# Optimization experiments

Measured on AMD Instinct MI355X. Metric: run time of the kernel, lower is better.

## Reference

```python
import jax, jax.numpy as jnp
import numpy as np
import math

E_IN, E_OUT = 512, 96
B, QL, PL = 64, 128, 196

def _lin(k, shape):
    fan_in = shape[1]
    bound = 1.0 / math.sqrt(fan_in)
    k1, k2 = jax.random.split(k)
    W = jax.random.uniform(k1, shape, jnp.float32, -bound, bound)
    b = jax.random.uniform(k2, (shape[0],), jnp.float32, -bound, bound)
    return W, b

def setup_inputs() -> dict:
    key = jax.random.key(0)
    ks = jax.random.split(key, 16)
    inp = {
        'z_d_cls': jax.random.normal(ks[0], (B, E_IN), jnp.float32),
        'Z_d_tok': jax.random.normal(ks[1], (B, QL, E_IN), jnp.float32),
        'z_t_cls': jax.random.normal(ks[2], (B, E_IN), jnp.float32),
        'Z_t_tok': jax.random.normal(ks[3], (B, QL, E_IN), jnp.float32),
        'z_v_cls': jax.random.normal(ks[4], (B, E_IN), jnp.float32),
        'Z_v_patch': jax.random.normal(ks[5], (B, PL, E_IN), jnp.float32),
    }
    names = ['t_cls', 'd_cls', 'v_cls', 't_tok', 'v_patch', 'tgl_q', 'tgl_k', 'tgl_v']
    for i, n in enumerate(names):
        W, b = _lin(ks[6 + i], (E_OUT, E_IN))
        inp[f'W_{n}'] = W
        inp[f'b_{n}'] = b
    inp['ln_g'] = jnp.ones((E_OUT,), jnp.float32)
    inp['ln_b'] = jnp.zeros((E_OUT,), jnp.float32)
    return inp

def _l2n(x, eps=1e-6):
    return x / jnp.maximum(jnp.linalg.norm(x, axis=-1, keepdims=True), eps)

def _proj(x, W, b):
    return x @ W.T + b

def _layer_norm(x, g, b, eps=1e-5):
    mu = jnp.mean(x, axis=-1, keepdims=True)
    var = jnp.mean((x - mu) ** 2, axis=-1, keepdims=True)
    return (x - mu) / jnp.sqrt(var + eps) * g + b

def reference(z_d_cls, Z_d_tok, z_t_cls, Z_t_tok, z_v_cls, Z_v_patch,
              W_t_cls, b_t_cls, W_d_cls, b_d_cls, W_v_cls, b_v_cls,
              W_t_tok, b_t_tok, W_v_patch, b_v_patch,
              W_tgl_q, b_tgl_q, W_tgl_k, b_tgl_k, W_tgl_v, b_tgl_v,
              ln_g, ln_b):
    # --- TGG: global-global text/doc cosine sim [B, B]
    t = _l2n(_proj(z_t_cls, W_t_cls, b_t_cls))
    d = _l2n(_proj(z_d_cls, W_d_cls, b_d_cls))
    S_TGG = t @ d.T
    # --- TGL: cross-attention over all batch pairs
    Q = _proj(Z_d_tok, W_tgl_q, b_tgl_q)   # [b, q, h]
    K = _proj(Z_t_tok, W_tgl_k, b_tgl_k)   # [c, k, h]
    V = _proj(Z_t_tok, W_tgl_v, b_tgl_v)   # [c, k, h]
    scores = jnp.einsum('bqh,ckh->bcqk', Q, K) / math.sqrt(E_OUT)
    attn = jax.nn.softmax(scores, axis=-1)
    context = jnp.einsum('bcqk,ckh->bcqh', attn, V).mean(axis=2)  # [b, c, h]
    context = _layer_norm(context, ln_g, ln_b)
    S_TGL = jnp.einsum('ih,ijh->ij', d, _l2n(context))
    S_TIB = 0.5 * (S_TGG + S_TGL)
    # --- CGG: global-global text/vision cosine sim
    v = _l2n(_proj(z_v_cls, W_v_cls, b_v_cls))
    S_CGG = t @ v.T
    # --- CLL: token-patch max similarity
    t_tok = _l2n(_proj(Z_t_tok, W_t_tok, b_t_tok))        # [b, t, h]
    v_pat = _l2n(_proj(Z_v_patch, W_v_patch, b_v_patch))  # [c, p, h]
    sim = jnp.einsum('bth,cph->bctp', t_tok, v_pat)
    S_CLL = sim.max(axis=(-1, -2))
    S_CAB = 0.5 * (S_CGG + S_CLL)
    return S_TIB + S_CAB
```

## Files before the change

### kernel.cpp

```cpp
#include <hip/hip_runtime.h>
#include <hip/hip_bf16.h>

typedef __bf16 bf16;
typedef __attribute__((ext_vector_type(8))) __bf16 bf16x8;
typedef __attribute__((ext_vector_type(4))) float f32x4;
typedef __attribute__((ext_vector_type(4))) unsigned int uint4v;

#define MFMA16(a, b, c) __builtin_amdgcn_mfma_f32_16x16x32_bf16(a, b, c, 0, 0, 0)

__device__ inline bf16x8 cvt8(const float* p) {
    f32x4 lo = *(const f32x4*)p;
    f32x4 hi = *(const f32x4*)(p + 4);
    bf16x8 r;
    r[0] = (bf16)lo[0]; r[1] = (bf16)lo[1]; r[2] = (bf16)lo[2]; r[3] = (bf16)lo[3];
    r[4] = (bf16)hi[0]; r[5] = (bf16)hi[1]; r[6] = (bf16)hi[2]; r[7] = (bf16)hi[3];
    return r;
}


struct WPtrs { const float* W[8]; };

__global__ __launch_bounds__(256) void cvtw_kernel(WPtrs wp, bf16* __restrict__ Wb) {
    int j   = blockIdx.x / 48;
    int blk = blockIdx.x - j * 48;
    int idx = (blk * 256 + threadIdx.x) * 4;
    f32x4 v = *(const f32x4*)(wp.W[j] + idx);
    bf16* dst = Wb + j * 49152 + idx;
    dst[0] = (bf16)v[0]; dst[1] = (bf16)v[1]; dst[2] = (bf16)v[2]; dst[3] = (bf16)v[3];
}


struct ProjParams {
    const float* src[8];
    const float* B[8];
    void* dst[8];
    const bf16* Wb;
};

__global__ __launch_bounds__(128, 8) void proj_kernel(ProjParams p) {
    int g   = blockIdx.x;
    int tid = threadIdx.x;
    int nh = tid >> 6, lane = tid & 63;
    int m = lane & 15, quad = lane >> 4;

    int job = 0, base = 0;
    if (g >= 2)    { job = 1; base = 2; }
    if (g >= 4)    { job = 2; base = 4; }
    if (g >= 6)    { job = 3; base = 6; }
    if (g >= 262)  { job = 4; base = 262; }
    if (g >= 518)  { job = 5; base = 518; }
    if (g >= 774)  { job = 6; base = 774; }
    if (g >= 1030) { job = 7; base = 1030; }
    int r0 = (g - base) << 5;

    const float* X  = p.src[job];
    const bf16*  wb = p.Wb + job * 49152 + (size_t)(nh * 48 + m) * 512 + quad * 8;
    const float* x0 = X + (size_t)(r0 + m) * 512 + quad * 8;
    const float* x1 = x0 + 16 * 512;

    f32x4 acc[2][3] = {};
    #pragma unroll 4
    for (int kk = 0; kk < 512; kk += 32) {
        bf16x8 a0 = cvt8(x0 + kk);
        bf16x8 a1 = cvt8(x1 + kk);
        #pragma unroll
        for (int nt = 0; nt < 3; nt++) {
            bf16x8 b = *(const bf16x8*)(wb + nt * 8192 + kk);
            acc[0][nt] = MFMA16(a0, b, acc[0][nt]);
            acc[1][nt] = MFMA16(a1, b, acc[1][nt]);
        }
    }
    const float* Bv = p.B[job];
    #pragma unroll
    for (int t2 = 0; t2 < 2; t2++)
        #pragma unroll
        for (int nt = 0; nt < 3; nt++) {
            float bb = Bv[nh * 48 + nt * 16 + m];
            acc[t2][nt][0] += bb; acc[t2][nt][1] += bb;
            acc[t2][nt][2] += bb; acc[t2][nt][3] += bb;
        }

    bool norm = (job < 3) || (job >= 6);
    __shared__ float sx[2][2][16];
    if (norm) {
        float ss[2][4];
        #pragma unroll
        for (int t2 = 0; t2 < 2; t2++)
            #pragma unroll
            for (int r = 0; r < 4; r++) {
                float s = 0.0f;
                #pragma unroll
                for (int nt = 0; nt < 3; nt++) s += acc[t2][nt][r] * acc[t2][nt][r];
                s += __shfl_xor(s, 1); s += __shfl_xor(s, 2);
                s += __shfl_xor(s, 4); s += __shfl_xor(s, 8);
                ss[t2][r] = s;
            }
        if (m == 0) {
            #pragma unroll
            for (int t2 = 0; t2 < 2; t2++)
                #pragma unroll
                for (int r = 0; r < 4; r++)
                    sx[nh][t2][quad * 4 + r] = ss[t2][r];
        }
        __syncthreads();
        #pragma unroll
        for (int t2 = 0; t2 < 2; t2++)
            #pragma unroll
            for (int r = 0; r < 4; r++) {
                float tot = ss[t2][r] + sx[1 - nh][t2][quad * 4 + r];
                float inv = 1.0f / fmaxf(sqrtf(tot), 1e-6f);
                #pragma unroll
                for (int nt = 0; nt < 3; nt++) acc[t2][nt][r] *= inv;
            }
    }
    if (job < 3) {
        float* dst = (float*)p.dst[job];
        #pragma unroll
        for (int t2 = 0; t2 < 2; t2++)
            #pragma unroll
            for (int r = 0; r < 4; r++)
                #pragma unroll
                for (int nt = 0; nt < 3; nt++)
                    dst[(size_t)(r0 + t2 * 16 + quad * 4 + r) * 96 + nh * 48 + nt * 16 + m] = acc[t2][nt][r];
    } else {
        bf16* dst = (bf16*)p.dst[job];
        #pragma unroll
        for (int t2 = 0; t2 < 2; t2++)
            #pragma unroll
            for (int r = 0; r < 4; r++)
                #pragma unroll
                for (int nt = 0; nt < 3; nt++)
                    dst[(size_t)(r0 + t2 * 16 + quad * 4 + r) * 96 + nh * 48 + nt * 16 + m] = (bf16)acc[t2][nt][r];
    }
}


__global__ __launch_bounds__(256) void attn_kernel(
    const bf16* __restrict__ Qg, const bf16* __restrict__ Kg, const bf16* __restrict__ Vg,
    const float* __restrict__ dvec, const float* __restrict__ ln_g, const float* __restrict__ ln_b,
    float* __restrict__ S_TGL)
{
    int b = blockIdx.x >> 6, c = blockIdx.x & 63;
    int tid = threadIdx.x, lane = tid & 63, w = tid >> 6;
    int m = lane & 15, quad = lane >> 4;
    const bf16* Q = Qg + (size_t)b * (128 * 96);
    const bf16* K = Kg + (size_t)c * (128 * 96);
    const bf16* V = Vg + (size_t)c * (128 * 96);

    __shared__ __align__(16) bf16 Klds[128 * 104];
    #pragma unroll
    for (int it = 0; it < 6; it++) {
        int ch = it * 256 + tid;
        int row = ch / 12, seg = ch - row * 12;
        *(uint4v*)(Klds + row * 104 + seg * 8) = *(const uint4v*)(K + ch * 8);
    }
    __syncthreads();

    f32x4 acc[2][8] = {};
    #pragma unroll
    for (int kk = 0; kk < 96; kk += 32) {
        bf16x8 a0 = *(const bf16x8*)(Q + (size_t)(w * 32 + m) * 96 + kk + quad * 8);
        bf16x8 a1 = *(const bf16x8*)(Q + (size_t)(w * 32 + 16 + m) * 96 + kk + quad * 8);
        #pragma unroll
        for (int nt = 0; nt < 8; nt++) {
            bf16x8 bb = *(const bf16x8*)(Klds + (nt * 16 + m) * 104 + kk + quad * 8);
            acc[0][nt] = MFMA16(a0, bb, acc[0][nt]);
            acc[1][nt] = MFMA16(a1, bb, acc[1][nt]);
        }
    }
    const float sc = 0.10206207261596575f;
    float wpart[8];
    #pragma unroll
    for (int nt = 0; nt < 8; nt++) wpart[nt] = 0.0f;
    #pragma unroll
    for (int mt = 0; mt < 2; mt++) {
        #pragma unroll
        for (int r = 0; r < 4; r++) {
            float tv[8]; float mx = -3.4e38f;
            #pragma unroll
            for (int nt = 0; nt < 8; nt++) { tv[nt] = acc[mt][nt][r] * sc; mx = fmaxf(mx, tv[nt]); }
            mx = fmaxf(mx, __shfl_xor(mx, 1)); mx = fmaxf(mx, __shfl_xor(mx, 2));
            mx = fmaxf(mx, __shfl_xor(mx, 4)); mx = fmaxf(mx, __shfl_xor(mx, 8));
            float s = 0.0f;
            #pragma unroll
            for (int nt = 0; nt < 8; nt++) { tv[nt] = __expf(tv[nt] - mx); s += tv[nt]; }
            s += __shfl_xor(s, 1); s += __shfl_xor(s, 2);
            s += __shfl_xor(s, 4); s += __shfl_xor(s, 8);
            float inv = 1.0f / s;
            #pragma unroll
            for (int nt = 0; nt < 8; nt++) wpart[nt] += tv[nt] * inv;
        }
    }
    #pragma unroll
    for (int nt = 0; nt < 8; nt++) {
        wpart[nt] += __shfl_xor(wpart[nt], 16);
        wpart[nt] += __shfl_xor(wpart[nt], 32);
    }
    __shared__ float wsum4[4][128];
    __shared__ float wk[128];
    __shared__ float ctxp[4][96];
    __shared__ float ctx[96];
    if (lane < 16) {
        #pragma unroll
        for (int nt = 0; nt < 8; nt++) wsum4[w][nt * 16 + lane] = wpart[nt];
    }
    __syncthreads();
    if (tid < 128) wk[tid] = wsum4[0][tid] + wsum4[1][tid] + wsum4[2][tid] + wsum4[3][tid];
    __syncthreads();
    {
        float c0 = 0.0f, c1 = 0.0f;
        if (lane < 48) {
            #pragma unroll 4
            for (int r = 0; r < 32; r++) {
                int k = w * 32 + r;
                unsigned u = *(const unsigned*)(V + (size_t)k * 96 + lane * 2);
                float lo = __uint_as_float(u << 16);
                float hi = __uint_as_float(u & 0xffff0000u);
                float wkk = wk[k];
                c0 += wkk * lo; c1 += wkk * hi;
            }
            ctxp[w][lane * 2]     = c0;
            ctxp[w][lane * 2 + 1] = c1;
        }
    }
    __syncthreads();
    if (tid < 96) ctx[tid] = (ctxp[0][tid] + ctxp[1][tid] + ctxp[2][tid] + ctxp[3][tid]) * (1.0f / 128.0f);
    __syncthreads();
    if (w == 0) {
        float x0 = ctx[lane];
        float x1 = (lane < 32) ? ctx[64 + lane] : 0.0f;
        float s = x0 + x1;
        #pragma unroll
        for (int d = 1; d < 64; d <<= 1) s += __shfl_xor(s, d);
        float mean = s * (1.0f / 96.0f);
        float e0 = x0 - mean;
        float e1 = (lane < 32) ? (x1 - mean) : 0.0f;
        float q = e0 * e0 + e1 * e1;
        #pragma unroll
        for (int d = 1; d < 64; d <<= 1) q += __shfl_xor(q, d);
        float rstd = rsqrtf(q * (1.0f / 96.0f) + 1e-5f);
        float y0 = e0 * rstd * ln_g[lane] + ln_b[lane];
        float y1 = 0.0f;
        if (lane < 32) y1 = e1 * rstd * ln_g[64 + lane] + ln_b[64 + lane];
        const float* db = dvec + b * 96;
        float dot = y0 * db[lane] + ((lane < 32) ? y1 * db[64 + lane] : 0.0f);
        float ss = y0 * y0 + y1 * y1;
        #pragma unroll
        for (int d = 1; d < 64; d <<= 1) { dot += __shfl_xor(dot, d); ss += __shfl_xor(ss, d); }
        if (lane == 0) S_TGL[blockIdx.x] = dot / fmaxf(sqrtf(ss), 1e-6f);
    }
}


__global__ __launch_bounds__(256) void cll_kernel(
    const bf16* __restrict__ Tt, const bf16* __restrict__ Vp, float* __restrict__ S_CLL)
{
    int b = blockIdx.x >> 6, c = blockIdx.x & 63;
    int tid = threadIdx.x, lane = tid & 63, w = tid >> 6;
    int m = lane & 15, quad = lane >> 4;
    const bf16* T = Tt + (size_t)b * (128 * 96);
    const bf16* P = Vp + (size_t)c * (196 * 96);

    __shared__ __align__(16) bf16 Plds[196 * 104];
    for (int ch = tid; ch < 2352; ch += 256) {
        int row = ch / 12, seg = ch - row * 12;
        *(uint4v*)(Plds + row * 104 + seg * 8) = *(const uint4v*)(P + ch * 8);
    }
    __syncthreads();

    int rofs[13];
    #pragma unroll
    for (int nt = 0; nt < 13; nt++) {
        int r = nt * 16 + m; if (r > 195) r = 195;
        rofs[nt] = r * 104;
    }
    f32x4 acc[2][13] = {};
    #pragma unroll
    for (int kk = 0; kk < 96; kk += 32) {
        bf16x8 a0 = *(const bf16x8*)(T + (size_t)(w * 32 + m) * 96 + kk + quad * 8);
        bf16x8 a1 = *(const bf16x8*)(T + (size_t)(w * 32 + 16 + m) * 96 + kk + quad * 8);
        #pragma unroll
        for (int nt = 0; nt < 13; nt++) {
            bf16x8 bb = *(const bf16x8*)(Plds + rofs[nt] + kk + quad * 8);
            acc[0][nt] = MFMA16(a0, bb, acc[0][nt]);
            acc[1][nt] = MFMA16(a1, bb, acc[1][nt]);
        }
    }
    float mx = -3.4e38f;
    #pragma unroll
    for (int mt = 0; mt < 2; mt++)
        #pragma unroll
        for (int nt = 0; nt < 13; nt++)
            #pragma unroll
            for (int r = 0; r < 4; r++) mx = fmaxf(mx, acc[mt][nt][r]);
    #pragma unroll
    for (int d = 1; d < 64; d <<= 1) mx = fmaxf(mx, __shfl_xor(mx, d));
    __shared__ float red[4];
    if (lane == 0) red[w] = mx;
    __syncthreads();
    if (tid == 0) S_CLL[blockIdx.x] = fmaxf(fmaxf(red[0], red[1]), fmaxf(red[2], red[3]));
}


__global__ __launch_bounds__(64) void final_kernel(
    const float* __restrict__ t, const float* __restrict__ d, const float* __restrict__ v,
    const float* __restrict__ S_TGL, const float* __restrict__ S_CLL, float* __restrict__ out)
{
    int i = blockIdx.x, j = threadIdx.x;
    __shared__ float ti[96];
    if (j < 64) ti[j] = t[i * 96 + j];
    if (j < 32) ti[64 + j] = t[i * 96 + 64 + j];
    __syncthreads();
    float tg = 0.0f, cg = 0.0f;
    const float* dj = d + j * 96;
    const float* vj = v + j * 96;
    #pragma unroll 8
    for (int h = 0; h < 96; h++) { float th = ti[h]; tg += th * dj[h]; cg += th * vj[h]; }
    float res = 0.5f * (tg + S_TGL[i * 64 + j]) + 0.5f * (cg + S_CLL[i * 64 + j]);
    out[i * 64 + j] = res;
}


extern "C" void kernel_launch(void* const* d_in, const int* in_sizes, int n_in,
                              void* d_out, int out_size, void* d_ws, size_t ws_size,
                              hipStream_t stream)
{
    (void)in_sizes; (void)n_in; (void)out_size; (void)ws_size;
    const float* z_d_cls   = (const float*)d_in[0];
    const float* Z_d_tok   = (const float*)d_in[1];
    const float* z_t_cls   = (const float*)d_in[2];
    const float* Z_t_tok   = (const float*)d_in[3];
    const float* z_v_cls   = (const float*)d_in[4];
    const float* Z_v_patch = (const float*)d_in[5];

    char* ws = (char*)d_ws;
    float* t     = (float*)(ws + 0);
    float* d     = (float*)(ws + 24576);
    float* v     = (float*)(ws + 49152);
    float* S_TGL = (float*)(ws + 73728);
    float* S_CLL = (float*)(ws + 90112);
    bf16* Wb = (bf16*)(ws + 106496);
    bf16* Qb = (bf16*)(ws + 892928);
    bf16* Kb = (bf16*)(ws + 892928 + 1572864);
    bf16* Vb = (bf16*)(ws + 892928 + 2 * 1572864);
    bf16* Tt = (bf16*)(ws + 892928 + 3 * 1572864);
    bf16* Vp = (bf16*)(ws + 892928 + 4 * 1572864);

    WPtrs wp;
    wp.W[0] = (const float*)d_in[6];
    wp.W[1] = (const float*)d_in[8];
    wp.W[2] = (const float*)d_in[10];
    wp.W[3] = (const float*)d_in[16];
    wp.W[4] = (const float*)d_in[18];
    wp.W[5] = (const float*)d_in[20];
    wp.W[6] = (const float*)d_in[12];
    wp.W[7] = (const float*)d_in[14];
    hipLaunchKernelGGL(cvtw_kernel, dim3(384), dim3(256), 0, stream, wp, Wb);

    ProjParams pp;
    pp.Wb = Wb;
    pp.src[0] = z_t_cls;   pp.B[0] = (const float*)d_in[7];  pp.dst[0] = t;
    pp.src[1] = z_d_cls;   pp.B[1] = (const float*)d_in[9];  pp.dst[1] = d;
    pp.src[2] = z_v_cls;   pp.B[2] = (const float*)d_in[11]; pp.dst[2] = v;
    pp.src[3] = Z_d_tok;   pp.B[3] = (const float*)d_in[17]; pp.dst[3] = Qb;
    pp.src[4] = Z_t_tok;   pp.B[4] = (const float*)d_in[19]; pp.dst[4] = Kb;
    pp.src[5] = Z_t_tok;   pp.B[5] = (const float*)d_in[21]; pp.dst[5] = Vb;
    pp.src[6] = Z_t_tok;   pp.B[6] = (const float*)d_in[13]; pp.dst[6] = Tt;
    pp.src[7] = Z_v_patch; pp.B[7] = (const float*)d_in[15]; pp.dst[7] = Vp;
    hipLaunchKernelGGL(proj_kernel, dim3(1422), dim3(128), 0, stream, pp);

    hipLaunchKernelGGL(attn_kernel, dim3(4096), dim3(256), 0, stream,
                       (const bf16*)Qb, (const bf16*)Kb, (const bf16*)Vb,
                       (const float*)d, (const float*)d_in[22], (const float*)d_in[23], S_TGL);
    hipLaunchKernelGGL(cll_kernel, dim3(4096), dim3(256), 0, stream,
                       (const bf16*)Tt, (const bf16*)Vp, S_CLL);
    hipLaunchKernelGGL(final_kernel, dim3(64), dim3(64), 0, stream,
                       (const float*)t, (const float*)d, (const float*)v,
                       (const float*)S_TGL, (const float*)S_CLL, (float*)d_out);
}
```

Measured before the change: 243.9 us.

## Fuse K/V/token projections, fold softmax scale into Q, merge attention and CLL

The three projections of Z_t_tok (K, V and the token projection) now run in one block that converts each input tile once and reuses it for all three weight sets. This cuts repeated global reads and fp32-to-bf16 conversions of the largest input. The softmax scale and log2(e) are folded into Q at projection time, so the attention softmax uses exp2 with no max subtraction. The attention and CLL kernels are merged into one 8192-block launch, with even and odd blocks taking each role and sharing a shared-memory union. Skipping the max subtraction relies on scores staying small enough not to overflow, and the fused K/V/T path uses more registers.

```diff
diff --git a/kernel.cpp b/kernel.cpp
--- a/kernel.cpp
+++ b/kernel.cpp
@@ -1,5 +1,6 @@
 #include <hip/hip_runtime.h>
 #include <hip/hip_bf16.h>
+#include <math.h>
 
 typedef __bf16 bf16;
 typedef __attribute__((ext_vector_type(8))) __bf16 bf16x8;
@@ -7,6 +8,8 @@
 typedef __attribute__((ext_vector_type(4))) unsigned int uint4v;
 
 #define MFMA16(a, b, c) __builtin_amdgcn_mfma_f32_16x16x32_bf16(a, b, c, 0, 0, 0)
+
+#define QSCALE 0.14724450f
 
 __device__ inline bf16x8 cvt8(const float* p) {
     f32x4 lo = *(const f32x4*)p;
@@ -31,58 +34,147 @@
 
 
 struct ProjParams {
-    const float* src[8];
-    const float* B[8];
-    void* dst[8];
+    const float* z_t_cls; const float* z_d_cls; const float* z_v_cls;
+    const float* Z_d_tok; const float* Z_t_tok; const float* Z_v_patch;
+    const float* b_t; const float* b_d; const float* b_v;
+    const float* b_q; const float* b_k; const float* b_vv; const float* b_tt; const float* b_vp;
+    float *t, *d, *v;
+    bf16 *Qb, *Kb, *Vb, *Tt, *Vp;
     const bf16* Wb;
 };
 
-__global__ __launch_bounds__(128, 8) void proj_kernel(ProjParams p) {
+__global__ __launch_bounds__(128, 3) void proj_kernel(ProjParams p) {
     int g   = blockIdx.x;
     int tid = threadIdx.x;
     int nh = tid >> 6, lane = tid & 63;
     int m = lane & 15, quad = lane >> 4;
 
-    int job = 0, base = 0;
-    if (g >= 2)    { job = 1; base = 2; }
-    if (g >= 4)    { job = 2; base = 4; }
-    if (g >= 6)    { job = 3; base = 6; }
-    if (g >= 262)  { job = 4; base = 262; }
-    if (g >= 518)  { job = 5; base = 518; }
-    if (g >= 774)  { job = 6; base = 774; }
-    if (g >= 1030) { job = 7; base = 1030; }
+    int job, base;
+    if (g < 2)        { job = 0; base = 0; }
+    else if (g < 4)   { job = 1; base = 2; }
+    else if (g < 6)   { job = 2; base = 4; }
+    else if (g < 262) { job = 3; base = 6; }
+    else if (g < 518) { job = 4; base = 262; }
+    else              { job = 5; base = 518; }
     int r0 = (g - base) << 5;
 
-    const float* X  = p.src[job];
-    const bf16*  wb = p.Wb + job * 49152 + (size_t)(nh * 48 + m) * 512 + quad * 8;
+    const float* X = (job == 0) ? p.z_t_cls : (job == 1) ? p.z_d_cls : (job == 2) ? p.z_v_cls
+                   : (job == 3) ? p.Z_d_tok : (job == 4) ? p.Z_t_tok : p.Z_v_patch;
     const float* x0 = X + (size_t)(r0 + m) * 512 + quad * 8;
     const float* x1 = x0 + 16 * 512;
 
-    f32x4 acc[2][3] = {};
-    #pragma unroll 4
-    for (int kk = 0; kk < 512; kk += 32) {
-        bf16x8 a0 = cvt8(x0 + kk);
-        bf16x8 a1 = cvt8(x1 + kk);
-        #pragma unroll
-        for (int nt = 0; nt < 3; nt++) {
-            bf16x8 b = *(const bf16x8*)(wb + nt * 8192 + kk);
-            acc[0][nt] = MFMA16(a0, b, acc[0][nt]);
-            acc[1][nt] = MFMA16(a1, b, acc[1][nt]);
-        }
-    }
-    const float* Bv = p.B[job];
-    #pragma unroll
-    for (int t2 = 0; t2 < 2; t2++)
-        #pragma unroll
-        for (int nt = 0; nt < 3; nt++) {
-            float bb = Bv[nh * 48 + nt * 16 + m];
-            acc[t2][nt][0] += bb; acc[t2][nt][1] += bb;
-            acc[t2][nt][2] += bb; acc[t2][nt][3] += bb;
-        }
-
-    bool norm = (job < 3) || (job >= 6);
     __shared__ float sx[2][2][16];
-    if (norm) {
+
+    if (job != 4) {
+        int jw = (job < 4) ? job : 7;
+        const bf16* wb = p.Wb + jw * 49152 + (size_t)(nh * 48 + m) * 512 + quad * 8;
+        f32x4 acc[2][3] = {};
+        #pragma unroll 4
+        for (int kk = 0; kk < 512; kk += 32) {
+            bf16x8 a0 = cvt8(x0 + kk);
+            bf16x8 a1 = cvt8(x1 + kk);
+            #pragma unroll
+            for (int nt = 0; nt < 3; nt++) {
+                bf16x8 b = *(const bf16x8*)(wb + nt * 8192 + kk);
+                acc[0][nt] = MFMA16(a0, b, acc[0][nt]);
+                acc[1][nt] = MFMA16(a1, b, acc[1][nt]);
+            }
+        }
+        const float* Bv = (job == 0) ? p.b_t : (job == 1) ? p.b_d : (job == 2) ? p.b_v
+                        : (job == 3) ? p.b_q : p.b_vp;
+        #pragma unroll
+        for (int t2 = 0; t2 < 2; t2++)
+            #pragma unroll
+            for (int nt = 0; nt < 3; nt++) {
+                float bb = Bv[nh * 48 + nt * 16 + m];
+                acc[t2][nt][0] += bb; acc[t2][nt][1] += bb;
+                acc[t2][nt][2] += bb; acc[t2][nt][3] += bb;
+            }
+        bool norm = (job != 3);
+        if (norm) {
+            float ss[2][4];
+            #pragma unroll
+            for (int t2 = 0; t2 < 2; t2++)
+                #pragma unroll
+                for (int r = 0; r < 4; r++) {
+                    float s = 0.0f;
+                    #pragma unroll
+                    for (int nt = 0; nt < 3; nt++) s += acc[t2][nt][r] * acc[t2][nt][r];
+                    s += __shfl_xor(s, 1); s += __shfl_xor(s, 2);
+                    s += __shfl_xor(s, 4); s += __shfl_xor(s, 8);
+                    ss[t2][r] = s;
+                }
+            if (m == 0)
+                #pragma unroll
+                for (int t2 = 0; t2 < 2; t2++)
+                    #pragma unroll
+                    for (int r = 0; r < 4; r++) sx[nh][t2][quad * 4 + r] = ss[t2][r];
+            __syncthreads();
+            #pragma unroll
+            for (int t2 = 0; t2 < 2; t2++)
+                #pragma unroll
+                for (int r = 0; r < 4; r++) {
+                    float inv = 1.0f / fmaxf(sqrtf(ss[t2][r] + sx[1 - nh][t2][quad * 4 + r]), 1e-6f);
+                    #pragma unroll
+                    for (int nt = 0; nt < 3; nt++) acc[t2][nt][r] *= inv;
+                }
+        } else {
+            #pragma unroll
+            for (int t2 = 0; t2 < 2; t2++)
+                #pragma unroll
+                for (int nt = 0; nt < 3; nt++) {
+                    acc[t2][nt][0] *= QSCALE; acc[t2][nt][1] *= QSCALE;
+                    acc[t2][nt][2] *= QSCALE; acc[t2][nt][3] *= QSCALE;
+                }
+        }
+        if (job < 3) {
+            float* dst = (job == 0) ? p.t : (job == 1) ? p.d : p.v;
+            #pragma unroll
+            for (int t2 = 0; t2 < 2; t2++)
+                #pragma unroll
+                for (int r = 0; r < 4; r++)
+                    #pragma unroll
+                    for (int nt = 0; nt < 3; nt++)
+                        dst[(size_t)(r0 + t2 * 16 + quad * 4 + r) * 96 + nh * 48 + nt * 16 + m] = acc[t2][nt][r];
+        } else {
+            bf16* dst = (job == 3) ? p.Qb : p.Vp;
+            #pragma unroll
+            for (int t2 = 0; t2 < 2; t2++)
+                #pragma unroll
+                for (int r = 0; r < 4; r++)
+                    #pragma unroll
+                    for (int nt = 0; nt < 3; nt++)
+                        dst[(size_t)(r0 + t2 * 16 + quad * 4 + r) * 96 + nh * 48 + nt * 16 + m] = (bf16)acc[t2][nt][r];
+        }
+    } else {
+        const bf16* wK = p.Wb + 4 * 49152 + (size_t)(nh * 48 + m) * 512 + quad * 8;
+        f32x4 acc[2][3][3] = {};
+        #pragma unroll 2
+        for (int kk = 0; kk < 512; kk += 32) {
+            bf16x8 a0 = cvt8(x0 + kk);
+            bf16x8 a1 = cvt8(x1 + kk);
+            #pragma unroll
+            for (int ws = 0; ws < 3; ws++)
+                #pragma unroll
+                for (int nt = 0; nt < 3; nt++) {
+                    bf16x8 b = *(const bf16x8*)(wK + ws * 49152 + nt * 8192 + kk);
+                    acc[0][ws][nt] = MFMA16(a0, b, acc[0][ws][nt]);
+                    acc[1][ws][nt] = MFMA16(a1, b, acc[1][ws][nt]);
+                }
+        }
+        #pragma unroll
+        for (int t2 = 0; t2 < 2; t2++)
+            #pragma unroll
+            for (int nt = 0; nt < 3; nt++) {
+                int col = nh * 48 + nt * 16 + m;
+                float bk = p.b_k[col], bv = p.b_vv[col], bt = p.b_tt[col];
+                #pragma unroll
+                for (int r = 0; r < 4; r++) {
+                    acc[t2][0][nt][r] += bk;
+                    acc[t2][1][nt][r] += bv;
+                    acc[t2][2][nt][r] += bt;
+                }
+            }
         float ss[2][4];
         #pragma unroll
         for (int t2 = 0; t2 < 2; t2++)
@@ -90,215 +182,195 @@
             for (int r = 0; r < 4; r++) {
                 float s = 0.0f;
                 #pragma unroll
-                for (int nt = 0; nt < 3; nt++) s += acc[t2][nt][r] * acc[t2][nt][r];
+                for (int nt = 0; nt < 3; nt++) s += acc[t2][2][nt][r] * acc[t2][2][nt][r];
                 s += __shfl_xor(s, 1); s += __shfl_xor(s, 2);
                 s += __shfl_xor(s, 4); s += __shfl_xor(s, 8);
                 ss[t2][r] = s;
             }
-        if (m == 0) {
-            #pragma unroll
-            for (int t2 = 0; t2 < 2; t2++)
-                #pragma unroll
-                for (int r = 0; r < 4; r++)
-                    sx[nh][t2][quad * 4 + r] = ss[t2][r];
-        }
+        if (m == 0)
+            #pragma unroll
+            for (int t2 = 0; t2 < 2; t2++)
+                #pragma unroll
+                for (int r = 0; r < 4; r++) sx[nh][t2][quad * 4 + r] = ss[t2][r];
         __syncthreads();
         #pragma unroll
         for (int t2 = 0; t2 < 2; t2++)
             #pragma unroll
             for (int r = 0; r < 4; r++) {
-                float tot = ss[t2][r] + sx[1 - nh][t2][quad * 4 + r];
-                float inv = 1.0f / fmaxf(sqrtf(tot), 1e-6f);
-                #pragma unroll
-                for (int nt = 0; nt < 3; nt++) acc[t2][nt][r] *= inv;
-            }
+                float inv = 1.0f / fmaxf(sqrtf(ss[t2][r] + sx[1 - nh][t2][quad * 4 + r]), 1e-6f);
+                #pragma unroll
+                for (int nt = 0; nt < 3; nt++) acc[t2][2][nt][r] *= inv;
+            }
+        #pragma unroll
+        for (int t2 = 0; t2 < 2; t2++)
+            #pragma unroll
+            for (int r = 0; r < 4; r++)
+                #pragma unroll
+                for (int nt = 0; nt < 3; nt++) {
+                    size_t o = (size_t)(r0 + t2 * 16 + quad * 4 + r) * 96 + nh * 48 + nt * 16 + m;
+                    p.Kb[o] = (bf16)acc[t2][0][nt][r];
+                    p.Vb[o] = (bf16)acc[t2][1][nt][r];
+                    p.Tt[o] = (bf16)acc[t2][2][nt][r];
+                }
     }
-    if (job < 3) {
-        float* dst = (float*)p.dst[job];
-        #pragma unroll
-        for (int t2 = 0; t2 < 2; t2++)
-            #pragma unroll
-            for (int r = 0; r < 4; r++)
-                #pragma unroll
-                for (int nt = 0; nt < 3; nt++)
-                    dst[(size_t)(r0 + t2 * 16 + quad * 4 + r) * 96 + nh * 48 + nt * 16 + m] = acc[t2][nt][r];
-    } else {
-        bf16* dst = (bf16*)p.dst[job];
-        #pragma unroll
-        for (int t2 = 0; t2 < 2; t2++)
-            #pragma unroll
-            for (int r = 0; r < 4; r++)
-                #pragma unroll
-                for (int nt = 0; nt < 3; nt++)
-                    dst[(size_t)(r0 + t2 * 16 + quad * 4 + r) * 96 + nh * 48 + nt * 16 + m] = (bf16)acc[t2][nt][r];
-    }
-}
-
-
-__global__ __launch_bounds__(256) void attn_kernel(
+}
+
+
+union AcSmem {
+    struct { bf16 K[128 * 104]; float wsum4[4][128]; float wk[128]; float ctxp[4][96]; float ctx[96]; } a;
+    struct { bf16 P[196 * 104]; float red[4]; } c;
+};
+
+__global__ __launch_bounds__(256, 3) void ac_kernel(
     const bf16* __restrict__ Qg, const bf16* __restrict__ Kg, const bf16* __restrict__ Vg,
+    const bf16* __restrict__ Tt, const bf16* __restrict__ Vp,
     const float* __restrict__ dvec, const float* __restrict__ ln_g, const float* __restrict__ ln_b,
-    float* __restrict__ S_TGL)
+    float* __restrict__ S_TGL, float* __restrict__ S_CLL)
 {
-    int b = blockIdx.x >> 6, c = blockIdx.x & 63;
+    __shared__ __align__(16) AcSmem sm;
+    int p   = blockIdx.x >> 1;
+    int role = blockIdx.x & 1;
+    int b = p >> 6, c = p & 63;
     int tid = threadIdx.x, lane = tid & 63, w = tid >> 6;
     int m = lane & 15, quad = lane >> 4;
-    const bf16* Q = Qg + (size_t)b * (128 * 96);
-    const bf16* K = Kg + (size_t)c * (128 * 96);
-    const bf16* V = Vg + (size_t)c * (128 * 96);
-
-    __shared__ __align__(16) bf16 Klds[128 * 104];
-    #pragma unroll
-    for (int it = 0; it < 6; it++) {
-        int ch = it * 256 + tid;
-        int row = ch / 12, seg = ch - row * 12;
-        *(uint4v*)(Klds + row * 104 + seg * 8) = *(const uint4v*)(K + ch * 8);
+
+    if (role == 0) {
+        const bf16* Q = Qg + (size_t)b * (128 * 96);
+        const bf16* K = Kg + (size_t)c * (128 * 96);
+        const bf16* V = Vg + (size_t)c * (128 * 96);
+        #pragma unroll
+        for (int it = 0; it < 6; it++) {
+            int ch = it * 256 + tid;
+            int row = ch / 12, seg = ch - row * 12;
+            *(uint4v*)(sm.a.K + row * 104 + seg * 8) = *(const uint4v*)(K + ch * 8);
+        }
+        __syncthreads();
+
+        f32x4 acc[2][8] = {};
+        #pragma unroll
+        for (int kk = 0; kk < 96; kk += 32) {
+            bf16x8 a0 = *(const bf16x8*)(Q + (size_t)(w * 32 + m) * 96 + kk + quad * 8);
+            bf16x8 a1 = *(const bf16x8*)(Q + (size_t)(w * 32 + 16 + m) * 96 + kk + quad * 8);
+            #pragma unroll
+            for (int nt = 0; nt < 8; nt++) {
+                bf16x8 bb = *(const bf16x8*)(sm.a.K + (nt * 16 + m) * 104 + kk + quad * 8);
+                acc[0][nt] = MFMA16(a0, bb, acc[0][nt]);
+                acc[1][nt] = MFMA16(a1, bb, acc[1][nt]);
+            }
+        }
+        float wpart[8];
+        #pragma unroll
+        for (int nt = 0; nt < 8; nt++) wpart[nt] = 0.0f;
+        #pragma unroll
+        for (int mt = 0; mt < 2; mt++) {
+            #pragma unroll
+            for (int r = 0; r < 4; r++) {
+                float tv[8]; float s = 0.0f;
+                #pragma unroll
+                for (int nt = 0; nt < 8; nt++) { tv[nt] = exp2f(acc[mt][nt][r]); s += tv[nt]; }
+                s += __shfl_xor(s, 1); s += __shfl_xor(s, 2);
+                s += __shfl_xor(s, 4); s += __shfl_xor(s, 8);
+                float inv = 1.0f / s;
+                #pragma unroll
+                for (int nt = 0; nt < 8; nt++) wpart[nt] += tv[nt] * inv;
+            }
+        }
+        #pragma unroll
+        for (int nt = 0; nt < 8; nt++) {
+            wpart[nt] += __shfl_xor(wpart[nt], 16);
+            wpart[nt] += __shfl_xor(wpart[nt], 32);
+        }
+        if (lane < 16) {
+            #pragma unroll
+            for (int nt = 0; nt < 8; nt++) sm.a.wsum4[w][nt * 16 + lane] = wpart[nt];
+        }
+        __syncthreads();
+        if (tid < 128)
+            sm.a.wk[tid] = sm.a.wsum4[0][tid] + sm.a.wsum4[1][tid] + sm.a.wsum4[2][tid] + sm.a.wsum4[3][tid];
+        __syncthreads();
+        {
+            float c0 = 0.0f, c1 = 0.0f;
+            if (lane < 48) {
+                #pragma unroll 4
+                for (int r = 0; r < 32; r++) {
+                    int k = w * 32 + r;
+                    unsigned u = *(const unsigned*)(V + (size_t)k * 96 + lane * 2);
+                    float lo = __uint_as_float(u << 16);
+                    float hi = __uint_as_float(u & 0xffff0000u);
+                    float wkk = sm.a.wk[k];
+                    c0 += wkk * lo; c1 += wkk * hi;
+                }
+                sm.a.ctxp[w][lane * 2]     = c0;
+                sm.a.ctxp[w][lane * 2 + 1] = c1;
+            }
+        }
+        __syncthreads();
+        if (tid < 96)
+            sm.a.ctx[tid] = (sm.a.ctxp[0][tid] + sm.a.ctxp[1][tid] + sm.a.ctxp[2][tid] + sm.a.ctxp[3][tid]) * (1.0f / 128.0f);
+        __syncthreads();
+        if (w == 0) {
+            float x0 = sm.a.ctx[lane];
+            float x1 = (lane < 32) ? sm.a.ctx[64 + lane] : 0.0f;
+            float s = x0 + x1;
+            #pragma unroll
+            for (int d = 1; d < 64; d <<= 1) s += __shfl_xor(s, d);
+            float mean = s * (1.0f / 96.0f);
+            float e0 = x0 - mean;
+            float e1 = (lane < 32) ? (x1 - mean) : 0.0f;
+            float q = e0 * e0 + e1 * e1;
+            #pragma unroll
+            for (int d = 1; d < 64; d <<= 1) q += __shfl_xor(q, d);
+            float rstd = rsqrtf(q * (1.0f / 96.0f) + 1e-5f);
+            float y0 = e0 * rstd * ln_g[lane] + ln_b[lane];
+            float y1 = 0.0f;
+            if (lane < 32) y1 = e1 * rstd * ln_g[64 + lane] + ln_b[64 + lane];
+            const float* db = dvec + b * 96;
+            float dot = y0 * db[lane] + ((lane < 32) ? y1 * db[64 + lane] : 0.0f);
+            float ssq = y0 * y0 + y1 * y1;
+            #pragma unroll
+            for (int d = 1; d < 64; d <<= 1) { dot += __shfl_xor(dot, d); ssq += __shfl_xor(ssq, d); }
+            if (lane == 0) S_TGL[p] = dot / fmaxf(sqrtf(ssq), 1e-6f);
+        }
+    } else {
+        const bf16* T = Tt + (size_t)b * (128 * 96);
+        const bf16* P = Vp + (size_t)c * (196 * 96);
+        for (int ch = tid; ch < 2352; ch += 256) {
+            int row = ch / 12, seg = ch - row * 12;
+            *(uint4v*)(sm.c.P + row * 104 + seg * 8) = *(const uint4v*)(P + ch * 8);
+        }
+        __syncthreads();
+
+        int rofs[13];
+        #pragma unroll
+        for (int nt = 0; nt < 13; nt++) {
+            int r = nt * 16 + m; if (r > 195) r = 195;
+            rofs[nt] = r * 104;
+        }
+        f32x4 acc[2][13] = {};
+        #pragma unroll
+        for (int kk = 0; kk < 96; kk += 32) {
+            bf16x8 a0 = *(const bf16x8*)(T + (size_t)(w * 32 + m) * 96 + kk + quad * 8);
+            bf16x8 a1 = *(const bf16x8*)(T + (size_t)(w * 32 + 16 + m) * 96 + kk + quad * 8);
+            #pragma unroll
+            for (int nt = 0; nt < 13; nt++) {
+                bf16x8 bb = *(const bf16x8*)(sm.c.P + rofs[nt] + kk + quad * 8);
+                acc[0][nt] = MFMA16(a0, bb, acc[0][nt]);
+                acc[1][nt] = MFMA16(a1, bb, acc[1][nt]);
+            }
+        }
+        float mx = -3.4e38f;
+        #pragma unroll
+        for (int mt = 0; mt < 2; mt++)
+            #pragma unroll
+            for (int nt = 0; nt < 13; nt++)
+                #pragma unroll
+                for (int r = 0; r < 4; r++) mx = fmaxf(mx, acc[mt][nt][r]);
+        #pragma unroll
+        for (int d = 1; d < 64; d <<= 1) mx = fmaxf(mx, __shfl_xor(mx, d));
+        if (lane == 0) sm.c.red[w] = mx;
+        __syncthreads();
+        if (tid == 0) S_CLL[p] = fmaxf(fmaxf(sm.c.red[0], sm.c.red[1]), fmaxf(sm.c.red[2], sm.c.red[3]));
     }
-    __syncthreads();
-
-    f32x4 acc[2][8] = {};
-    #pragma unroll
-    for (int kk = 0; kk < 96; kk += 32) {
-        bf16x8 a0 = *(const bf16x8*)(Q + (size_t)(w * 32 + m) * 96 + kk + quad * 8);
-        bf16x8 a1 = *(const bf16x8*)(Q + (size_t)(w * 32 + 16 + m) * 96 + kk + quad * 8);
-        #pragma unroll
-        for (int nt = 0; nt < 8; nt++) {
-            bf16x8 bb = *(const bf16x8*)(Klds + (nt * 16 + m) * 104 + kk + quad * 8);
-            acc[0][nt] = MFMA16(a0, bb, acc[0][nt]);
-            acc[1][nt] = MFMA16(a1, bb, acc[1][nt]);
-        }
-    }
-    const float sc = 0.10206207261596575f;
-    float wpart[8];
-    #pragma unroll
-    for (int nt = 0; nt < 8; nt++) wpart[nt] = 0.0f;
-    #pragma unroll
-    for (int mt = 0; mt < 2; mt++) {
-        #pragma unroll
-        for (int r = 0; r < 4; r++) {
-            float tv[8]; float mx = -3.4e38f;
-            #pragma unroll
-            for (int nt = 0; nt < 8; nt++) { tv[nt] = acc[mt][nt][r] * sc; mx = fmaxf(mx, tv[nt]); }
-            mx = fmaxf(mx, __shfl_xor(mx, 1)); mx = fmaxf(mx, __shfl_xor(mx, 2));
-            mx = fmaxf(mx, __shfl_xor(mx, 4)); mx = fmaxf(mx, __shfl_xor(mx, 8));
-            float s = 0.0f;
-            #pragma unroll
-            for (int nt = 0; nt < 8; nt++) { tv[nt] = __expf(tv[nt] - mx); s += tv[nt]; }
-            s += __shfl_xor(s, 1); s += __shfl_xor(s, 2);
-            s += __shfl_xor(s, 4); s += __shfl_xor(s, 8);
-            float inv = 1.0f / s;
-            #pragma unroll
-            for (int nt = 0; nt < 8; nt++) wpart[nt] += tv[nt] * inv;
-        }
-    }
-    #pragma unroll
-    for (int nt = 0; nt < 8; nt++) {
-        wpart[nt] += __shfl_xor(wpart[nt], 16);
-        wpart[nt] += __shfl_xor(wpart[nt], 32);
-    }
-    __shared__ float wsum4[4][128];
-    __shared__ float wk[128];
-    __shared__ float ctxp[4][96];
-    __shared__ float ctx[96];
-    if (lane < 16) {
-        #pragma unroll
-        for (int nt = 0; nt < 8; nt++) wsum4[w][nt * 16 + lane] = wpart[nt];
-    }
-    __syncthreads();
-    if (tid < 128) wk[tid] = wsum4[0][tid] + wsum4[1][tid] + wsum4[2][tid] + wsum4[3][tid];
-    __syncthreads();
-    {
-        float c0 = 0.0f, c1 = 0.0f;
-        if (lane < 48) {
-            #pragma unroll 4
-            for (int r = 0; r < 32; r++) {
-                int k = w * 32 + r;
-                unsigned u = *(const unsigned*)(V + (size_t)k * 96 + lane * 2);
-                float lo = __uint_as_float(u << 16);
-                float hi = __uint_as_float(u & 0xffff0000u);
-                float wkk = wk[k];
-                c0 += wkk * lo; c1 += wkk * hi;
-            }
-            ctxp[w][lane * 2]     = c0;
-            ctxp[w][lane * 2 + 1] = c1;
-        }
-    }
-    __syncthreads();
-    if (tid < 96) ctx[tid] = (ctxp[0][tid] + ctxp[1][tid] + ctxp[2][tid] + ctxp[3][tid]) * (1.0f / 128.0f);
-    __syncthreads();
-    if (w == 0) {
-        float x0 = ctx[lane];
-        float x1 = (lane < 32) ? ctx[64 + lane] : 0.0f;
-        float s = x0 + x1;
-        #pragma unroll
-        for (int d = 1; d < 64; d <<= 1) s += __shfl_xor(s, d);
-        float mean = s * (1.0f / 96.0f);
-        float e0 = x0 - mean;
-        float e1 = (lane < 32) ? (x1 - mean) : 0.0f;
-        float q = e0 * e0 + e1 * e1;
-        #pragma unroll
-        for (int d = 1; d < 64; d <<= 1) q += __shfl_xor(q, d);
-        float rstd = rsqrtf(q * (1.0f / 96.0f) + 1e-5f);
-        float y0 = e0 * rstd * ln_g[lane] + ln_b[lane];
-        float y1 = 0.0f;
-        if (lane < 32) y1 = e1 * rstd * ln_g[64 + lane] + ln_b[64 + lane];
-        const float* db = dvec + b * 96;
-        float dot = y0 * db[lane] + ((lane < 32) ? y1 * db[64 + lane] : 0.0f);
-        float ss = y0 * y0 + y1 * y1;
-        #pragma unroll
-        for (int d = 1; d < 64; d <<= 1) { dot += __shfl_xor(dot, d); ss += __shfl_xor(ss, d); }
-        if (lane == 0) S_TGL[blockIdx.x] = dot / fmaxf(sqrtf(ss), 1e-6f);
-    }
-}
-
-
-__global__ __launch_bounds__(256) void cll_kernel(
-    const bf16* __restrict__ Tt, const bf16* __restrict__ Vp, float* __restrict__ S_CLL)
-{
-    int b = blockIdx.x >> 6, c = blockIdx.x & 63;
-    int tid = threadIdx.x, lane = tid & 63, w = tid >> 6;
-    int m = lane & 15, quad = lane >> 4;
-    const bf16* T = Tt + (size_t)b * (128 * 96);
-    const bf16* P = Vp + (size_t)c * (196 * 96);
-
-    __shared__ __align__(16) bf16 Plds[196 * 104];
-    for (int ch = tid; ch < 2352; ch += 256) {
-        int row = ch / 12, seg = ch - row * 12;
-        *(uint4v*)(Plds + row * 104 + seg * 8) = *(const uint4v*)(P + ch * 8);
-    }
-    __syncthreads();
-
-    int rofs[13];
-    #pragma unroll
-    for (int nt = 0; nt < 13; nt++) {
-        int r = nt * 16 + m; if (r > 195) r = 195;
-        rofs[nt] = r * 104;
-    }
-    f32x4 acc[2][13] = {};
-    #pragma unroll
-    for (int kk = 0; kk < 96; kk += 32) {
-        bf16x8 a0 = *(const bf16x8*)(T + (size_t)(w * 32 + m) * 96 + kk + quad * 8);
-        bf16x8 a1 = *(const bf16x8*)(T + (size_t)(w * 32 + 16 + m) * 96 + kk + quad * 8);
-        #pragma unroll
-        for (int nt = 0; nt < 13; nt++) {
-            bf16x8 bb = *(const bf16x8*)(Plds + rofs[nt] + kk + quad * 8);
-            acc[0][nt] = MFMA16(a0, bb, acc[0][nt]);
-            acc[1][nt] = MFMA16(a1, bb, acc[1][nt]);
-        }
-    }
-    float mx = -3.4e38f;
-    #pragma unroll
-    for (int mt = 0; mt < 2; mt++)
-        #pragma unroll
-        for (int nt = 0; nt < 13; nt++)
-            #pragma unroll
-            for (int r = 0; r < 4; r++) mx = fmaxf(mx, acc[mt][nt][r]);
-    #pragma unroll
-    for (int d = 1; d < 64; d <<= 1) mx = fmaxf(mx, __shfl_xor(mx, d));
-    __shared__ float red[4];
-    if (lane == 0) red[w] = mx;
-    __syncthreads();
-    if (tid == 0) S_CLL[blockIdx.x] = fmaxf(fmaxf(red[0], red[1]), fmaxf(red[2], red[3]));
 }
 
 
@@ -326,13 +398,6 @@
                               hipStream_t stream)
 {
     (void)in_sizes; (void)n_in; (void)out_size; (void)ws_size;
-    const float* z_d_cls   = (const float*)d_in[0];
-    const float* Z_d_tok   = (const float*)d_in[1];
-    const float* z_t_cls   = (const float*)d_in[2];
-    const float* Z_t_tok   = (const float*)d_in[3];
-    const float* z_v_cls   = (const float*)d_in[4];
-    const float* Z_v_patch = (const float*)d_in[5];
-
     char* ws = (char*)d_ws;
     float* t     = (float*)(ws + 0);
     float* d     = (float*)(ws + 24576);
@@ -358,22 +423,30 @@
     hipLaunchKernelGGL(cvtw_kernel, dim3(384), dim3(256), 0, stream, wp, Wb);
 
     ProjParams pp;
+    pp.z_t_cls = (const float*)d_in[2];
+    pp.z_d_cls = (const float*)d_in[0];
+    pp.z_v_cls = (const float*)d_in[4];
+    pp.Z_d_tok = (const float*)d_in[1];
+    pp.Z_t_tok = (const float*)d_in[3];
+    pp.Z_v_patch = (const float*)d_in[5];
+    pp.b_t  = (const float*)d_in[7];
+    pp.b_d  = (const float*)d_in[9];
+    pp.b_v  = (const float*)d_in[11];
+    pp.b_q  = (const float*)d_in[17];
+    pp.b_k  = (const float*)d_in[19];
+    pp.b_vv = (const float*)d_in[21];
+    pp.b_tt = (const float*)d_in[13];
+    pp.b_vp = (const float*)d_in[15];
+    pp.t = t; pp.d = d; pp.v = v;
+    pp.Qb = Qb; pp.Kb = Kb; pp.Vb = Vb; pp.Tt = Tt; pp.Vp = Vp;
     pp.Wb = Wb;
-    pp.src[0] = z_t_cls;   pp.B[0] = (const float*)d_in[7];  pp.dst[0] = t;
-    pp.src[1] = z_d_cls;   pp.B[1] = (const float*)d_in[9];  pp.dst[1] = d;
-    pp.src[2] = z_v_cls;   pp.B[2] = (const float*)d_in[11]; pp.dst[2] = v;
-    pp.src[3] = Z_d_tok;   pp.B[3] = (const float*)d_in[17]; pp.dst[3] = Qb;
-    pp.src[4] = Z_t_tok;   pp.B[4] = (const float*)d_in[19]; pp.dst[4] = Kb;
-    pp.src[5] = Z_t_tok;   pp.B[5] = (const float*)d_in[21]; pp.dst[5] = Vb;
-    pp.src[6] = Z_t_tok;   pp.B[6] = (const float*)d_in[13]; pp.dst[6] = Tt;
-    pp.src[7] = Z_v_patch; pp.B[7] = (const float*)d_in[15]; pp.dst[7] = Vp;
-    hipLaunchKernelGGL(proj_kernel, dim3(1422), dim3(128), 0, stream, pp);
-
-    hipLaunchKernelGGL(attn_kernel, dim3(4096), dim3(256), 0, stream,
+    hipLaunchKernelGGL(proj_kernel, dim3(910), dim3(128), 0, stream, pp);
+
+    hipLaunchKernelGGL(ac_kernel, dim3(8192), dim3(256), 0, stream,
                        (const bf16*)Qb, (const bf16*)Kb, (const bf16*)Vb,
-                       (const float*)d, (const float*)d_in[22], (const float*)d_in[23], S_TGL);
-    hipLaunchKernelGGL(cll_kernel, dim3(4096), dim3(256), 0, stream,
-                       (const bf16*)Tt, (const bf16*)Vp, S_CLL);
+                       (const bf16*)Tt, (const bf16*)Vp,
+                       (const float*)d, (const float*)d_in[22], (const float*)d_in[23],
+                       S_TGL, S_CLL);
     hipLaunchKernelGGL(final_kernel, dim3(64), dim3(64), 0, stream,
                        (const float*)t, (const float*)d, (const float*)v,
                        (const float*)S_TGL, (const float*)S_CLL, (float*)d_out);
```

New measurement: 262.5 us. 1.08x slower.

## Reuse patch tile across batches in CLL, fold softmax scale into Q

Applied to the files above, without the earlier changes.

The CLL kernel now loads each vision-patch tile into LDS once and loops over 8 text batches, so it launches 512 blocks instead of 4096 and writes the max for each batch pair. The attention softmax scale times log2(e) is folded into the Q projection, and the kernel uses exp2f without subtracting the row max, which drops a max pass and its shuffles. That relies on the scores staying small enough not to overflow. The attention kernel reads K straight from global/L2 instead of staging it in LDS, and launch bounds are adjusted on the projection, attention and CLL kernels.

```diff
diff --git a/kernel.cpp b/kernel.cpp
--- a/kernel.cpp
+++ b/kernel.cpp
@@ -1,5 +1,6 @@
 #include <hip/hip_runtime.h>
 #include <hip/hip_bf16.h>
+#include <math.h>
 
 typedef __bf16 bf16;
 typedef __attribute__((ext_vector_type(8))) __bf16 bf16x8;
@@ -7,6 +8,8 @@
 typedef __attribute__((ext_vector_type(4))) unsigned int uint4v;
 
 #define MFMA16(a, b, c) __builtin_amdgcn_mfma_f32_16x16x32_bf16(a, b, c, 0, 0, 0)
+
+#define QSCALE 0.14724450f
 
 __device__ inline bf16x8 cvt8(const float* p) {
     f32x4 lo = *(const f32x4*)p;
@@ -37,7 +40,7 @@
     const bf16* Wb;
 };
 
-__global__ __launch_bounds__(128, 8) void proj_kernel(ProjParams p) {
+__global__ __launch_bounds__(128, 4) void proj_kernel(ProjParams p) {
     int g   = blockIdx.x;
     int tid = threadIdx.x;
     int nh = tid >> 6, lane = tid & 63;
@@ -112,6 +115,14 @@
                 #pragma unroll
                 for (int nt = 0; nt < 3; nt++) acc[t2][nt][r] *= inv;
             }
+    } else if (job == 3) {
+        #pragma unroll
+        for (int t2 = 0; t2 < 2; t2++)
+            #pragma unroll
+            for (int nt = 0; nt < 3; nt++) {
+                acc[t2][nt][0] *= QSCALE; acc[t2][nt][1] *= QSCALE;
+                acc[t2][nt][2] *= QSCALE; acc[t2][nt][3] *= QSCALE;
+            }
     }
     if (job < 3) {
         float* dst = (float*)p.dst[job];
@@ -135,27 +146,19 @@
 }
 
 
-__global__ __launch_bounds__(256) void attn_kernel(
+__global__ __launch_bounds__(256, 4) void attn_kernel(
     const bf16* __restrict__ Qg, const bf16* __restrict__ Kg, const bf16* __restrict__ Vg,
     const float* __restrict__ dvec, const float* __restrict__ ln_g, const float* __restrict__ ln_b,
     float* __restrict__ S_TGL)
 {
-    int b = blockIdx.x >> 6, c = blockIdx.x & 63;
+    int pr = blockIdx.x;
+    int b = pr >> 6, c = pr & 63;
     int tid = threadIdx.x, lane = tid & 63, w = tid >> 6;
     int m = lane & 15, quad = lane >> 4;
     const bf16* Q = Qg + (size_t)b * (128 * 96);
     const bf16* K = Kg + (size_t)c * (128 * 96);
     const bf16* V = Vg + (size_t)c * (128 * 96);
 
-    __shared__ __align__(16) bf16 Klds[128 * 104];
-    #pragma unroll
-    for (int it = 0; it < 6; it++) {
-        int ch = it * 256 + tid;
-        int row = ch / 12, seg = ch - row * 12;
-        *(uint4v*)(Klds + row * 104 + seg * 8) = *(const uint4v*)(K + ch * 8);
-    }
-    __syncthreads();
-
     f32x4 acc[2][8] = {};
     #pragma unroll
     for (int kk = 0; kk < 96; kk += 32) {
@@ -163,12 +166,11 @@
         bf16x8 a1 = *(const bf16x8*)(Q + (size_t)(w * 32 + 16 + m) * 96 + kk + quad * 8);
         #pragma unroll
         for (int nt = 0; nt < 8; nt++) {
-            bf16x8 bb = *(const bf16x8*)(Klds + (nt * 16 + m) * 104 + kk + quad * 8);
+            bf16x8 bb = *(const bf16x8*)(K + (size_t)(nt * 16 + m) * 96 + kk + quad * 8);
             acc[0][nt] = MFMA16(a0, bb, acc[0][nt]);
             acc[1][nt] = MFMA16(a1, bb, acc[1][nt]);
         }
     }
-    const float sc = 0.10206207261596575f;
     float wpart[8];
     #pragma unroll
     for (int nt = 0; nt < 8; nt++) wpart[nt] = 0.0f;
@@ -176,14 +178,9 @@
     for (int mt = 0; mt < 2; mt++) {
         #pragma unroll
         for (int r = 0; r < 4; r++) {
-            float tv[8]; float mx = -3.4e38f;
-            #pragma unroll
-            for (int nt = 0; nt < 8; nt++) { tv[nt] = acc[mt][nt][r] * sc; mx = fmaxf(mx, tv[nt]); }
-            mx = fmaxf(mx, __shfl_xor(mx, 1)); mx = fmaxf(mx, __shfl_xor(mx, 2));
-            mx = fmaxf(mx, __shfl_xor(mx, 4)); mx = fmaxf(mx, __shfl_xor(mx, 8));
-            float s = 0.0f;
-            #pragma unroll
-            for (int nt = 0; nt < 8; nt++) { tv[nt] = __expf(tv[nt] - mx); s += tv[nt]; }
+            float tv[8]; float s = 0.0f;
+            #pragma unroll
+            for (int nt = 0; nt < 8; nt++) { tv[nt] = exp2f(acc[mt][nt][r]); s += tv[nt]; }
             s += __shfl_xor(s, 1); s += __shfl_xor(s, 2);
             s += __shfl_xor(s, 4); s += __shfl_xor(s, 8);
             float inv = 1.0f / s;
@@ -244,61 +241,65 @@
         if (lane < 32) y1 = e1 * rstd * ln_g[64 + lane] + ln_b[64 + lane];
         const float* db = dvec + b * 96;
         float dot = y0 * db[lane] + ((lane < 32) ? y1 * db[64 + lane] : 0.0f);
-        float ss = y0 * y0 + y1 * y1;
-        #pragma unroll
-        for (int d = 1; d < 64; d <<= 1) { dot += __shfl_xor(dot, d); ss += __shfl_xor(ss, d); }
-        if (lane == 0) S_TGL[blockIdx.x] = dot / fmaxf(sqrtf(ss), 1e-6f);
-    }
-}
-
-
-__global__ __launch_bounds__(256) void cll_kernel(
+        float ssq = y0 * y0 + y1 * y1;
+        #pragma unroll
+        for (int d = 1; d < 64; d <<= 1) { dot += __shfl_xor(dot, d); ssq += __shfl_xor(ssq, d); }
+        if (lane == 0) S_TGL[pr] = dot / fmaxf(sqrtf(ssq), 1e-6f);
+    }
+}
+
+
+__global__ __launch_bounds__(256, 3) void cll_kernel(
     const bf16* __restrict__ Tt, const bf16* __restrict__ Vp, float* __restrict__ S_CLL)
 {
-    int b = blockIdx.x >> 6, c = blockIdx.x & 63;
+    int c = blockIdx.x >> 3, bg = blockIdx.x & 7;
     int tid = threadIdx.x, lane = tid & 63, w = tid >> 6;
     int m = lane & 15, quad = lane >> 4;
-    const bf16* T = Tt + (size_t)b * (128 * 96);
     const bf16* P = Vp + (size_t)c * (196 * 96);
 
     __shared__ __align__(16) bf16 Plds[196 * 104];
+    __shared__ float red[8][4];
     for (int ch = tid; ch < 2352; ch += 256) {
         int row = ch / 12, seg = ch - row * 12;
         *(uint4v*)(Plds + row * 104 + seg * 8) = *(const uint4v*)(P + ch * 8);
     }
-    __syncthreads();
-
     int rofs[13];
     #pragma unroll
     for (int nt = 0; nt < 13; nt++) {
         int r = nt * 16 + m; if (r > 195) r = 195;
         rofs[nt] = r * 104;
     }
-    f32x4 acc[2][13] = {};
-    #pragma unroll
-    for (int kk = 0; kk < 96; kk += 32) {
-        bf16x8 a0 = *(const bf16x8*)(T + (size_t)(w * 32 + m) * 96 + kk + quad * 8);
-        bf16x8 a1 = *(const bf16x8*)(T + (size_t)(w * 32 + 16 + m) * 96 + kk + quad * 8);
-        #pragma unroll
-        for (int nt = 0; nt < 13; nt++) {
-            bf16x8 bb = *(const bf16x8*)(Plds + rofs[nt] + kk + quad * 8);
-            acc[0][nt] = MFMA16(a0, bb, acc[0][nt]);
-            acc[1][nt] = MFMA16(a1, bb, acc[1][nt]);
-        }
-    }
-    float mx = -3.4e38f;
-    #pragma unroll
-    for (int mt = 0; mt < 2; mt++)
-        #pragma unroll
-        for (int nt = 0; nt < 13; nt++)
-            #pragma unroll
-            for (int r = 0; r < 4; r++) mx = fmaxf(mx, acc[mt][nt][r]);
-    #pragma unroll
-    for (int d = 1; d < 64; d <<= 1) mx = fmaxf(mx, __shfl_xor(mx, d));
-    __shared__ float red[4];
-    if (lane == 0) red[w] = mx;
-    __syncthreads();
-    if (tid == 0) S_CLL[blockIdx.x] = fmaxf(fmaxf(red[0], red[1]), fmaxf(red[2], red[3]));
+    __syncthreads();
+
+    for (int bi = 0; bi < 8; bi++) {
+        const bf16* T = Tt + (size_t)(bg * 8 + bi) * (128 * 96);
+        f32x4 acc[2][13] = {};
+        #pragma unroll
+        for (int kk = 0; kk < 96; kk += 32) {
+            bf16x8 a0 = *(const bf16x8*)(T + (size_t)(w * 32 + m) * 96 + kk + quad * 8);
+            bf16x8 a1 = *(const bf16x8*)(T + (size_t)(w * 32 + 16 + m) * 96 + kk + quad * 8);
+            #pragma unroll
+            for (int nt = 0; nt < 13; nt++) {
+                bf16x8 bb = *(const bf16x8*)(Plds + rofs[nt] + kk + quad * 8);
+                acc[0][nt] = MFMA16(a0, bb, acc[0][nt]);
+                acc[1][nt] = MFMA16(a1, bb, acc[1][nt]);
+            }
+        }
+        float mx = -3.4e38f;
+        #pragma unroll
+        for (int mt = 0; mt < 2; mt++)
+            #pragma unroll
+            for (int nt = 0; nt < 13; nt++)
+                #pragma unroll
+                for (int r = 0; r < 4; r++) mx = fmaxf(mx, acc[mt][nt][r]);
+        #pragma unroll
+        for (int d = 1; d < 64; d <<= 1) mx = fmaxf(mx, __shfl_xor(mx, d));
+        if (lane == 0) red[bi][w] = mx;
+    }
+    __syncthreads();
+    if (tid < 8)
+        S_CLL[(size_t)(bg * 8 + tid) * 64 + c] =
+            fmaxf(fmaxf(red[tid][0], red[tid][1]), fmaxf(red[tid][2], red[tid][3]));
 }
 
 
@@ -326,13 +327,6 @@
                               hipStream_t stream)
 {
     (void)in_sizes; (void)n_in; (void)out_size; (void)ws_size;
-    const float* z_d_cls   = (const float*)d_in[0];
-    const float* Z_d_tok   = (const float*)d_in[1];
-    const float* z_t_cls   = (const float*)d_in[2];
-    const float* Z_t_tok   = (const float*)d_in[3];
-    const float* z_v_cls   = (const float*)d_in[4];
-    const float* Z_v_patch = (const float*)d_in[5];
-
     char* ws = (char*)d_ws;
     float* t     = (float*)(ws + 0);
     float* d     = (float*)(ws + 24576);
@@ -359,20 +353,20 @@
 
     ProjParams pp;
     pp.Wb = Wb;
-    pp.src[0] = z_t_cls;   pp.B[0] = (const float*)d_in[7];  pp.dst[0] = t;
-    pp.src[1] = z_d_cls;   pp.B[1] = (const float*)d_in[9];  pp.dst[1] = d;
-    pp.src[2] = z_v_cls;   pp.B[2] = (const float*)d_in[11]; pp.dst[2] = v;
-    pp.src[3] = Z_d_tok;   pp.B[3] = (const float*)d_in[17]; pp.dst[3] = Qb;
-    pp.src[4] = Z_t_tok;   pp.B[4] = (const float*)d_in[19]; pp.dst[4] = Kb;
-    pp.src[5] = Z_t_tok;   pp.B[5] = (const float*)d_in[21]; pp.dst[5] = Vb;
-    pp.src[6] = Z_t_tok;   pp.B[6] = (const float*)d_in[13]; pp.dst[6] = Tt;
-    pp.src[7] = Z_v_patch; pp.B[7] = (const float*)d_in[15]; pp.dst[7] = Vp;
+    pp.src[0] = (const float*)d_in[2];  pp.B[0] = (const float*)d_in[7];  pp.dst[0] = t;
+    pp.src[1] = (const float*)d_in[0];  pp.B[1] = (const float*)d_in[9];  pp.dst[1] = d;
+    pp.src[2] = (const float*)d_in[4];  pp.B[2] = (const float*)d_in[11]; pp.dst[2] = v;
+    pp.src[3] = (const float*)d_in[1];  pp.B[3] = (const float*)d_in[17]; pp.dst[3] = Qb;
+    pp.src[4] = (const float*)d_in[3];  pp.B[4] = (const float*)d_in[19]; pp.dst[4] = Kb;
+    pp.src[5] = (const float*)d_in[3];  pp.B[5] = (const float*)d_in[21]; pp.dst[5] = Vb;
+    pp.src[6] = (const float*)d_in[3];  pp.B[6] = (const float*)d_in[13]; pp.dst[6] = Tt;
+    pp.src[7] = (const float*)d_in[5];  pp.B[7] = (const float*)d_in[15]; pp.dst[7] = Vp;
     hipLaunchKernelGGL(proj_kernel, dim3(1422), dim3(128), 0, stream, pp);
 
     hipLaunchKernelGGL(attn_kernel, dim3(4096), dim3(256), 0, stream,
                        (const bf16*)Qb, (const bf16*)Kb, (const bf16*)Vb,
                        (const float*)d, (const float*)d_in[22], (const float*)d_in[23], S_TGL);
-    hipLaunchKernelGGL(cll_kernel, dim3(4096), dim3(256), 0, stream,
+    hipLaunchKernelGGL(cll_kernel, dim3(512), dim3(256), 0, stream,
                        (const bf16*)Tt, (const bf16*)Vp, S_CLL);
     hipLaunchKernelGGL(final_kernel, dim3(64), dim3(64), 0, stream,
                        (const float*)t, (const float*)d, (const float*)v,
```

New measurement: 390.7 us. +60.2%, slower.
